# Kernel optimization log

Hardware: AMD Instinct MI355X
Metric: run time of the kernel (lower is better)

The kernel has to match this reference:

```python
import jax, jax.numpy as jnp
import numpy as np

S_LEN, T_LEN, BATCH, HID = 32, 32, 64, 512


def setup_inputs() -> dict:
    key = jax.random.key(0)
    ks = jax.random.split(key, 5)
    H = HID
    sc = lambda n: 1.0 / np.sqrt(n)
    return {
        "source": jax.random.normal(ks[0], (S_LEN, BATCH, H), jnp.float32),
        "target": jax.random.normal(ks[1], (T_LEN, BATCH, H), jnp.float32),
        # H2h Dense: concat(s_h, t_h) [B, 2H] -> [B, H], linear
        "W_H2h": (jax.random.normal(ks[2], (2 * H, H), jnp.float32) * sc(2 * H)),
        "b_H2h": jnp.zeros((H,), jnp.float32),
        # shared LSTMCell weights (Keras gate order i, f, g, o)
        "W_kernel": (jax.random.normal(ks[3], (H, 4 * H), jnp.float32) * sc(H)),
        "W_rec": (jax.random.normal(ks[4], (H, 4 * H), jnp.float32) * sc(H)),
        "b_lstm": jnp.zeros((4 * H,), jnp.float32),
    }


def _lstm_cell(x, h, c, Wk, Wr, b):
    # Keras LSTMCell math, gate order i, f, g(candidate), o
    z = x @ Wk + h @ Wr + b  # [B, 4H]
    i, f, g, o = jnp.split(z, 4, axis=-1)
    c2 = jax.nn.sigmoid(f) * c + jax.nn.sigmoid(i) * jnp.tanh(g)
    h2 = jax.nn.sigmoid(o) * jnp.tanh(c2)
    return h2, c2


def reference(source, target, W_H2h, b_H2h, W_kernel, W_rec, b_lstm):
    # source: [S, B, H] (time-major), target: [T, B, H]
    T, B, H = target.shape

    def inner(s_state, t_slice):
        # s_state carried along the target axis; t_slice is target cell j state
        s_step, s_h, s_m = s_state
        t_step, t_h, t_m = t_slice
        hmid = jnp.concatenate([s_h, t_h], axis=1) @ W_H2h + b_H2h  # [B, H]
        ns_h, ns_m = _lstm_cell(s_step, hmid, s_m, W_kernel, W_rec, b_lstm)
        nt_h, nt_m = _lstm_cell(t_step, hmid, t_m, W_kernel, W_rec, b_lstm)
        # step arrays get overwritten with the new hidden state
        return (ns_h, ns_h, ns_m), (nt_h, nt_h, nt_m)

    def outer(t_arrays, s_in):
        # fresh source state per outer step i: step = source[i], h = m = 0
        z = jnp.zeros_like(s_in)
        (s_step_f, _, _), t_new = jax.lax.scan(inner, (s_in, z, z), t_arrays)
        return t_new, s_step_f

    zeros = jnp.zeros((T, B, H), source.dtype)
    t_final, source_out = jax.lax.scan(outer, (target, zeros, zeros), source)
    return source_out, t_final[0]
```

## Files before the change

### kernel.cpp

```cpp
#include <hip/hip_runtime.h>

#define BLK 256

typedef __bf16 bf16;
typedef __bf16 bf16x8 __attribute__((ext_vector_type(8)));
typedef float f32x4 __attribute__((ext_vector_type(4)));

__device__ __forceinline__ float sigm(float x) { return 1.f / (1.f + __expf(-x)); }
__device__ __forceinline__ float tanh_(float x) {
    x = fminf(fmaxf(x, -15.f), 15.f);
    float e = __expf(2.f * x);
    return (e - 1.f) / (e + 1.f);
}

__device__ __forceinline__ void gl2lds(const bf16* g, bf16* l) {
    __builtin_amdgcn_global_load_lds((const __attribute__((address_space(1))) void*)g,
                                     (__attribute__((address_space(3))) void*)l, 16, 0, 0);
}

__global__ __launch_bounds__(256) void k_prep(
    const float* __restrict__ src, const float* __restrict__ tgt,
    const float* __restrict__ WH, const float* __restrict__ bH,
    const float* __restrict__ Wk, const float* __restrict__ Wr,
    const float* __restrict__ bl,
    bf16* __restrict__ srcb, bf16* __restrict__ tgtb,
    bf16* __restrict__ WHhi, bf16* __restrict__ WHlo,
    bf16* __restrict__ Wrhi, bf16* __restrict__ Wrlo,
    bf16* __restrict__ P2, float* __restrict__ bz) {
    __shared__ float tile[64][65];
    const int bid = blockIdx.x, t = threadIdx.x;
    if (bid < 512) {
        const float* in = (bid < 256) ? Wr : Wk;
        bf16* ohi = (bid < 256) ? Wrhi : P2;
        bf16* olo = (bid < 256) ? Wrlo : nullptr;
        const int b = bid & 255;
        const int tr = b >> 5, tc = b & 31;
#pragma unroll
        for (int q = 0; q < 16; q++) {
            int idx = q * 256 + t, lr = idx >> 6, lc = idx & 63;
            tile[lr][lc] = in[(size_t)(tr * 64 + lr) * 2048 + tc * 64 + lc];
        }
        __syncthreads();
#pragma unroll
        for (int q = 0; q < 16; q++) {
            int idx = q * 256 + t, lr = idx >> 6, lc = idx & 63;
            float v = tile[lc][lr];
            size_t o = (size_t)(tc * 64 + lr) * 512 + tr * 64 + lc;
            bf16 h = (bf16)v;
            ohi[o] = h;
            if (olo) olo[o] = (bf16)(v - (float)h);
        }
    } else if (bid < 520) {
        int c = (bid - 512) * 256 + t;
        float s = bl[c];
        for (int k = 0; k < 512; k++) s += bH[k] * Wr[(size_t)k * 2048 + c];
        bz[c] = s;
    } else {
        const int gt = (bid - 520) * 256 + t, NT = 504 * 256;
        for (int id = gt; id < 1048576; id += NT) srcb[id] = (bf16)src[id];
        for (int id = gt; id < 1048576; id += NT) tgtb[id] = (bf16)tgt[id];
        for (int id = gt; id < 524288; id += NT) {
            float v = WH[id];
            bf16 h = (bf16)v;
            WHhi[id] = h;
            WHlo[id] = (bf16)(v - (float)h);
        }
    }
}

__global__ __launch_bounds__(256, 4) void k_gemmP(
    const bf16* __restrict__ Wrhi, const bf16* __restrict__ Wrlo,
    const bf16* __restrict__ WHhi, const bf16* __restrict__ WHlo,
    bf16* __restrict__ P3, bf16* __restrict__ P4) {
    __shared__ __align__(16) bf16 At[64 * 64];
    __shared__ __align__(16) bf16 Bt[128 * 64];
    const int t = threadIdx.x, w = t >> 6, l = t & 63;
    const int m0 = (blockIdx.x >> 3) * 64, n0 = (blockIdx.x & 7) * 128;
    f32x4 acc[2][4] = {};
    const bf16* Aps[3] = {Wrhi, Wrlo, Wrhi};
    const bf16* Bps[3] = {WHhi, WHhi, WHlo};
    for (int ph = 0; ph < 3; ph++) {
        const bf16* Ap = Aps[ph] + (size_t)m0 * 512;
        const bf16* Bp = Bps[ph] + (size_t)n0 * 512;
        for (int kt = 0; kt < 8; kt++) {
            int k0 = kt * 64;
            __syncthreads();
#pragma unroll
            for (int q = 0; q < 2; q++) {
                int pp = q * 256 + t;
                int r = pp >> 3, c = (pp & 7) ^ (r & 7);
                gl2lds(Ap + (size_t)r * 512 + k0 + c * 8, &At[(q * 256 + w * 64) * 8]);
            }
#pragma unroll
            for (int q = 0; q < 4; q++) {
                int pp = q * 256 + t;
                int r = pp >> 3, c = (pp & 7) ^ (r & 7);
                gl2lds(Bp + (size_t)r * 512 + k0 + c * 8, &Bt[(q * 256 + w * 64) * 8]);
            }
            __syncthreads();
#pragma unroll
            for (int ks = 0; ks < 2; ks++) {
                int c = ks * 4 + (l >> 4);
                bf16x8 af[2], bb[4];
#pragma unroll
                for (int mt = 0; mt < 2; mt++) {
                    int r = (w >> 1) * 32 + mt * 16 + (l & 15);
                    af[mt] = *(const bf16x8*)&At[(r * 8 + (c ^ (r & 7))) * 8];
                }
#pragma unroll
                for (int g = 0; g < 4; g++) {
                    int r = g * 32 + (w & 1) * 16 + (l & 15);
                    bb[g] = *(const bf16x8*)&Bt[(r * 8 + (c ^ (r & 7))) * 8];
                }
#pragma unroll
                for (int mt = 0; mt < 2; mt++)
#pragma unroll
                    for (int g = 0; g < 4; g++)
                        acc[mt][g] = __builtin_amdgcn_mfma_f32_16x16x32_bf16(
                            af[mt], bb[g], acc[mt][g], 0, 0, 0);
            }
        }
    }
    const bool hihalf = (n0 >= 512);
#pragma unroll
    for (int mt = 0; mt < 2; mt++) {
#pragma unroll
        for (int g = 0; g < 4; g++) {
            int np = n0 + g * 32 + (w & 1) * 16 + (l & 15);
#pragma unroll
            for (int r = 0; r < 4; r++) {
                int c = m0 + (w >> 1) * 32 + mt * 16 + ((l >> 4) << 2) + r;
                float v = acc[mt][g][r];
                if (!hihalf) P4[(size_t)c * 512 + np] = (bf16)v;
                else P3[(size_t)c * 512 + (np - 512)] = (bf16)v;
            }
        }
    }
}

__global__ __launch_bounds__(256, 3) void k_diag7(
    int d, int i_lo, int Kd,
    const bf16* __restrict__ srcb, const bf16* __restrict__ tgtb,
    const bf16* __restrict__ P2, const bf16* __restrict__ P3,
    const bf16* __restrict__ P4,
    const float* __restrict__ bz,
    const bf16* __restrict__ shR, bf16* __restrict__ shW,
    const bf16* __restrict__ thR, bf16* __restrict__ thW,
    float* __restrict__ sc, float* __restrict__ tc,
    float* __restrict__ out) {
    __shared__ __align__(16) bf16 As[64 * 32];
    __shared__ __align__(16) bf16 At2[64 * 32];
    __shared__ __align__(16) bf16 Bk[128 * 32];
    __shared__ __align__(16) bf16 Bs[128 * 32];
    __shared__ __align__(16) bf16 Bt[128 * 32];
    const int t = threadIdx.x, w = t >> 6, l = t & 63;
    const int bid = blockIdx.x;
    const int xcd = bid & 7, idx = bid >> 3;
    const int ch0 = (xcd * 2 + (idx & 1)) << 5;
    const int cell = idx >> 1;
    const int i = i_lo + cell, j = d - i;
    const bool uS = (j > 0), uT = (i > 0);
    const size_t stI = (size_t)i * 32768, stJ = (size_t)j * 32768;

    const bf16* Asrc = (j == 0 ? srcb : shR) + stI;
    const bf16* Atsrc = (i == 0 ? tgtb : thR) + stJ;

    f32x4 accS[2][4] = {};
    f32x4 accT[2][4] = {};
    f32x4 accU[2][4] = {};

#pragma unroll 1
    for (int kt = 0; kt < 16; kt++) {
        const int k0 = kt * 32;
        __syncthreads();
        {
            int rA = t >> 2, cA = (t & 3) ^ (rA & 3);
            size_t soA = (size_t)rA * 512 + k0 + cA * 8;
            gl2lds(Asrc + soA, As + w * 512);
            gl2lds(Atsrc + soA, At2 + w * 512);
        }
#pragma unroll
        for (int q = 0; q < 2; q++) {
            int pp = q * 256 + t;
            int r = pp >> 2, c = (pp & 3) ^ (r & 3);
            size_t so = (size_t)((r >> 5) * 512 + ch0 + (r & 31)) * 512 + k0 + c * 8;
            int dsto = (q * 256 + w * 64) * 8;
            gl2lds(P2 + so, Bk + dsto);
            if (uS) gl2lds(P4 + so, Bs + dsto);
            if (uT) gl2lds(P3 + so, Bt + dsto);
        }
        __syncthreads();

        const int cq = l >> 4;
        bf16x8 aS[2], aT[2], bb[4];
#pragma unroll
        for (int mt = 0; mt < 2; mt++) {
            int r = (w >> 1) * 32 + mt * 16 + (l & 15);
            int co = (r * 4 + (cq ^ (r & 3))) * 8;
            aS[mt] = *(const bf16x8*)&As[co];
            aT[mt] = *(const bf16x8*)&At2[co];
        }
#pragma unroll
        for (int g = 0; g < 4; g++) {
            int r = g * 32 + (w & 1) * 16 + (l & 15);
            bb[g] = *(const bf16x8*)&Bk[(r * 4 + (cq ^ (r & 3))) * 8];
        }
#pragma unroll
        for (int mt = 0; mt < 2; mt++)
#pragma unroll
            for (int g = 0; g < 4; g++) {
                accS[mt][g] = __builtin_amdgcn_mfma_f32_16x16x32_bf16(
                    aS[mt], bb[g], accS[mt][g], 0, 0, 0);
                accT[mt][g] = __builtin_amdgcn_mfma_f32_16x16x32_bf16(
                    aT[mt], bb[g], accT[mt][g], 0, 0, 0);
            }
        if (uS) {
#pragma unroll
            for (int g = 0; g < 4; g++) {
                int r = g * 32 + (w & 1) * 16 + (l & 15);
                bb[g] = *(const bf16x8*)&Bs[(r * 4 + (cq ^ (r & 3))) * 8];
            }
#pragma unroll
            for (int mt = 0; mt < 2; mt++)
#pragma unroll
                for (int g = 0; g < 4; g++)
                    accU[mt][g] = __builtin_amdgcn_mfma_f32_16x16x32_bf16(
                        aS[mt], bb[g], accU[mt][g], 0, 0, 0);
        }
        if (uT) {
#pragma unroll
            for (int g = 0; g < 4; g++) {
                int r = g * 32 + (w & 1) * 16 + (l & 15);
                bb[g] = *(const bf16x8*)&Bt[(r * 4 + (cq ^ (r & 3))) * 8];
            }
#pragma unroll
            for (int mt = 0; mt < 2; mt++)
#pragma unroll
                for (int g = 0; g < 4; g++)
                    accU[mt][g] = __builtin_amdgcn_mfma_f32_16x16x32_bf16(
                        aT[mt], bb[g], accU[mt][g], 0, 0, 0);
        }
    }

    const int h = ch0 + (w & 1) * 16 + (l & 15);
    float bzv[4];
#pragma unroll
    for (int g = 0; g < 4; g++) bzv[g] = bz[g * 512 + h];
#pragma unroll
    for (int mt = 0; mt < 2; mt++) {
#pragma unroll
        for (int r = 0; r < 4; r++) {
            int b = (w >> 1) * 32 + mt * 16 + ((l >> 4) << 2) + r;
            float u0 = accU[mt][0][r], u1 = accU[mt][1][r];
            float u2 = accU[mt][2][r], u3 = accU[mt][3][r];
            {
                float zi = accS[mt][0][r] + u0 + bzv[0];
                float zf = accS[mt][1][r] + u1 + bzv[1];
                float zg = accS[mt][2][r] + u2 + bzv[2];
                float zo = accS[mt][3][r] + u3 + bzv[3];
                size_t off = stI + (size_t)b * 512 + h;
                float cold = uS ? sc[off] : 0.f;
                float c2 = sigm(zf) * cold + sigm(zi) * tanh_(zg);
                float h2 = sigm(zo) * tanh_(c2);
                sc[off] = c2;
                shW[off] = (bf16)h2;
                if (j == 31) out[off] = h2;
            }
            {
                float zi = accT[mt][0][r] + u0 + bzv[0];
                float zf = accT[mt][1][r] + u1 + bzv[1];
                float zg = accT[mt][2][r] + u2 + bzv[2];
                float zo = accT[mt][3][r] + u3 + bzv[3];
                size_t off = stJ + (size_t)b * 512 + h;
                float cold = uT ? tc[off] : 0.f;
                float c2 = sigm(zf) * cold + sigm(zi) * tanh_(zg);
                float h2 = sigm(zo) * tanh_(c2);
                tc[off] = c2;
                thW[off] = (bf16)h2;
                if (i == 31) out[1048576 + off] = h2;
            }
        }
    }
}


extern "C" void kernel_launch(void* const* d_in, const int* in_sizes, int n_in,
                              void* d_out, int out_size, void* d_ws, size_t ws_size,
                              hipStream_t stream) {
    char* w = (char*)d_ws;
    const size_t MB = 1u << 20;
    const float* src = (const float*)d_in[0];
    const float* tgt = (const float*)d_in[1];
    const float* WH = (const float*)d_in[2];
    const float* bH = (const float*)d_in[3];
    const float* Wk = (const float*)d_in[4];
    const float* Wr = (const float*)d_in[5];
    const float* bl = (const float*)d_in[6];
    float* out = (float*)d_out;

    bf16* srcb = (bf16*)(w + 0 * MB);
    bf16* tgtb = (bf16*)(w + 2 * MB);
    bf16* WHhi = (bf16*)(w + 4 * MB);
    bf16* WHlo = (bf16*)(w + 5 * MB);
    bf16* Wrhi = (bf16*)(w + 6 * MB);
    bf16* Wrlo = (bf16*)(w + 8 * MB);
    bf16* P2 = (bf16*)(w + 12 * MB);
    bf16* P3 = (bf16*)(w + 14 * MB);
    bf16* P4 = (bf16*)(w + 16 * MB);
    float* bz = (float*)(w + 20 * MB);
    bf16* sh = (bf16*)(w + 21 * MB);
    bf16* th = (bf16*)(w + 25 * MB);
    float* sc = (float*)(w + 29 * MB);
    float* tc = (float*)(w + 33 * MB);

    k_prep<<<1024, BLK, 0, stream>>>(src, tgt, WH, bH, Wk, Wr, bl, srcb, tgtb,
                                     WHhi, WHlo, Wrhi, Wrlo, P2, bz);
    k_gemmP<<<256, BLK, 0, stream>>>(Wrhi, Wrlo, WHhi, WHlo, P3, P4);

    for (int d = 0; d < 63; d++) {
        int i_lo = d > 31 ? d - 31 : 0;
        int i_hi = d < 31 ? d : 31;
        int Kd = i_hi - i_lo + 1;
        const bf16* shR = sh + (size_t)(d & 1) * 1048576;
        bf16* shW = sh + (size_t)((d + 1) & 1) * 1048576;
        const bf16* thR = th + (size_t)(d & 1) * 1048576;
        bf16* thW = th + (size_t)((d + 1) & 1) * 1048576;
        k_diag7<<<Kd * 16, BLK, 0, stream>>>(d, i_lo, Kd, srcb, tgtb, P2, P3, P4,
                                             bz, shR, shW, thR, thW, sc, tc, out);
    }
}
```

Measured before the change: 1.681 ms.

## Replace per-diagonal launches with persistent kernel using dataflow counters

The 63 per-diagonal kernel launches are replaced by one persistent kernel. It walks work items in wavefront order, and each item spin-waits on per-cell atomic counters until its source and target predecessors have finished. Counters are zeroed in the prep kernel, and the double-buffered hidden-state arrays are indexed by j and i parity rather than by diagonal. This aims to remove launch overhead and the global barrier between diagonals so cells can start as soon as their inputs are ready. The cost is spin-waiting, a risk of deadlock if not all blocks are resident, and possible hazards in reusing the ping-pong buffers.

New measurement: 2.925 ms. 1.74x slower.

```diff
diff --git a/kernel.cpp b/kernel.cpp
--- a/kernel.cpp
+++ b/kernel.cpp
@@ -1,6 +1,7 @@
 #include <hip/hip_runtime.h>
 
 #define BLK 256
+#define N_ITEMS 16384
 
 typedef __bf16 bf16;
 typedef __bf16 bf16x8 __attribute__((ext_vector_type(8)));
@@ -26,7 +27,7 @@
     bf16* __restrict__ srcb, bf16* __restrict__ tgtb,
     bf16* __restrict__ WHhi, bf16* __restrict__ WHlo,
     bf16* __restrict__ Wrhi, bf16* __restrict__ Wrlo,
-    bf16* __restrict__ P2, float* __restrict__ bz) {
+    bf16* __restrict__ P2, float* __restrict__ bz, int* __restrict__ cnt) {
     __shared__ float tile[64][65];
     const int bid = blockIdx.x, t = threadIdx.x;
     if (bid < 512) {
@@ -51,6 +52,8 @@
             if (olo) olo[o] = (bf16)(v - (float)h);
         }
     } else if (bid < 520) {
+        if (bid == 512)
+            for (int z = t; z < 1024; z += 256) cnt[z] = 0;
         int c = (bid - 512) * 256 + t;
         float s = bl[c];
         for (int k = 0; k < 512; k++) s += bH[k] * Wr[(size_t)k * 2048 + c];
@@ -138,148 +141,180 @@
     }
 }
 
-__global__ __launch_bounds__(256, 3) void k_diag7(
-    int d, int i_lo, int Kd,
+__global__ __launch_bounds__(256, 3) void k_persist(
     const bf16* __restrict__ srcb, const bf16* __restrict__ tgtb,
     const bf16* __restrict__ P2, const bf16* __restrict__ P3,
     const bf16* __restrict__ P4,
     const float* __restrict__ bz,
-    const bf16* __restrict__ shR, bf16* __restrict__ shW,
-    const bf16* __restrict__ thR, bf16* __restrict__ thW,
+    bf16* __restrict__ sh, bf16* __restrict__ th,
     float* __restrict__ sc, float* __restrict__ tc,
-    float* __restrict__ out) {
+    int* __restrict__ cnt, float* __restrict__ out) {
     __shared__ __align__(16) bf16 As[64 * 32];
     __shared__ __align__(16) bf16 At2[64 * 32];
     __shared__ __align__(16) bf16 Bk[128 * 32];
     __shared__ __align__(16) bf16 Bs[128 * 32];
     __shared__ __align__(16) bf16 Bt[128 * 32];
     const int t = threadIdx.x, w = t >> 6, l = t & 63;
-    const int bid = blockIdx.x;
-    const int xcd = bid & 7, idx = bid >> 3;
-    const int ch0 = (xcd * 2 + (idx & 1)) << 5;
-    const int cell = idx >> 1;
-    const int i = i_lo + cell, j = d - i;
-    const bool uS = (j > 0), uT = (i > 0);
-    const size_t stI = (size_t)i * 32768, stJ = (size_t)j * 32768;
-
-    const bf16* Asrc = (j == 0 ? srcb : shR) + stI;
-    const bf16* Atsrc = (i == 0 ? tgtb : thR) + stJ;
-
-    f32x4 accS[2][4] = {};
-    f32x4 accT[2][4] = {};
-    f32x4 accU[2][4] = {};
+    const int G = gridDim.x;
+
+    for (int item = blockIdx.x; item < N_ITEMS; item += G) {
+        const int c = item >> 4, ch0 = (item & 15) << 5;
+        int d = 0, st = 0, stPrev = 0;
+        for (;;) {
+            const int lo = d > 31 ? d - 31 : 0, hi = d < 31 ? d : 31;
+            const int Kd = hi - lo + 1;
+            if (c < st + Kd) break;
+            stPrev = st; st += Kd; ++d;
+        }
+        const int i = (d > 31 ? d - 31 : 0) + (c - st), j = d - i;
+        const bool uS = (j > 0), uT = (i > 0);
+
+        if (t == 0) {
+            const int lop = d > 32 ? d - 32 : 0;
+            if (uS) {
+                int* p = cnt + stPrev + (i - lop);
+                while (__hip_atomic_load(p, __ATOMIC_RELAXED, __HIP_MEMORY_SCOPE_AGENT) < 16)
+                    __builtin_amdgcn_s_sleep(2);
+                (void)__hip_atomic_load(p, __ATOMIC_ACQUIRE, __HIP_MEMORY_SCOPE_AGENT);
+            }
+            if (uT) {
+                int* p = cnt + stPrev + (i - 1 - lop);
+                while (__hip_atomic_load(p, __ATOMIC_RELAXED, __HIP_MEMORY_SCOPE_AGENT) < 16)
+                    __builtin_amdgcn_s_sleep(2);
+                (void)__hip_atomic_load(p, __ATOMIC_ACQUIRE, __HIP_MEMORY_SCOPE_AGENT);
+            }
+        }
+        __syncthreads();
+
+        const size_t stI = (size_t)i * 32768, stJ = (size_t)j * 32768;
+        const bf16* Asrc = (j == 0) ? srcb + stI
+                                    : sh + (size_t)((j & 1) ^ 1) * 1048576 + stI;
+        const bf16* Atsrc = (i == 0) ? tgtb + stJ
+                                     : th + (size_t)((i & 1) ^ 1) * 1048576 + stJ;
+        bf16* shW = sh + (size_t)(j & 1) * 1048576;
+        bf16* thW = th + (size_t)(i & 1) * 1048576;
+
+        f32x4 accS[2][4] = {};
+        f32x4 accT[2][4] = {};
+        f32x4 accU[2][4] = {};
 
 #pragma unroll 1
-    for (int kt = 0; kt < 16; kt++) {
-        const int k0 = kt * 32;
-        __syncthreads();
-        {
-            int rA = t >> 2, cA = (t & 3) ^ (rA & 3);
-            size_t soA = (size_t)rA * 512 + k0 + cA * 8;
-            gl2lds(Asrc + soA, As + w * 512);
-            gl2lds(Atsrc + soA, At2 + w * 512);
-        }
-#pragma unroll
-        for (int q = 0; q < 2; q++) {
-            int pp = q * 256 + t;
-            int r = pp >> 2, c = (pp & 3) ^ (r & 3);
-            size_t so = (size_t)((r >> 5) * 512 + ch0 + (r & 31)) * 512 + k0 + c * 8;
-            int dsto = (q * 256 + w * 64) * 8;
-            gl2lds(P2 + so, Bk + dsto);
-            if (uS) gl2lds(P4 + so, Bs + dsto);
-            if (uT) gl2lds(P3 + so, Bt + dsto);
-        }
-        __syncthreads();
-
-        const int cq = l >> 4;
-        bf16x8 aS[2], aT[2], bb[4];
-#pragma unroll
-        for (int mt = 0; mt < 2; mt++) {
-            int r = (w >> 1) * 32 + mt * 16 + (l & 15);
-            int co = (r * 4 + (cq ^ (r & 3))) * 8;
-            aS[mt] = *(const bf16x8*)&As[co];
-            aT[mt] = *(const bf16x8*)&At2[co];
-        }
-#pragma unroll
-        for (int g = 0; g < 4; g++) {
-            int r = g * 32 + (w & 1) * 16 + (l & 15);
-            bb[g] = *(const bf16x8*)&Bk[(r * 4 + (cq ^ (r & 3))) * 8];
-        }
-#pragma unroll
-        for (int mt = 0; mt < 2; mt++)
-#pragma unroll
-            for (int g = 0; g < 4; g++) {
-                accS[mt][g] = __builtin_amdgcn_mfma_f32_16x16x32_bf16(
-                    aS[mt], bb[g], accS[mt][g], 0, 0, 0);
-                accT[mt][g] = __builtin_amdgcn_mfma_f32_16x16x32_bf16(
-                    aT[mt], bb[g], accT[mt][g], 0, 0, 0);
-            }
-        if (uS) {
+        for (int kt = 0; kt < 16; kt++) {
+            const int k0 = kt * 32;
+            __syncthreads();
+            {
+                int rA = t >> 2, cA = (t & 3) ^ (rA & 3);
+                size_t soA = (size_t)rA * 512 + k0 + cA * 8;
+                gl2lds(Asrc + soA, As + w * 512);
+                gl2lds(Atsrc + soA, At2 + w * 512);
+            }
+#pragma unroll
+            for (int q = 0; q < 2; q++) {
+                int pp = q * 256 + t;
+                int r = pp >> 2, cc = (pp & 3) ^ (r & 3);
+                size_t so = (size_t)((r >> 5) * 512 + ch0 + (r & 31)) * 512 + k0 + cc * 8;
+                int dsto = (q * 256 + w * 64) * 8;
+                gl2lds(P2 + so, Bk + dsto);
+                if (uS) gl2lds(P4 + so, Bs + dsto);
+                if (uT) gl2lds(P3 + so, Bt + dsto);
+            }
+            __syncthreads();
+
+            const int cq = l >> 4;
+            bf16x8 aS[2], aT[2], bb[4];
+#pragma unroll
+            for (int mt = 0; mt < 2; mt++) {
+                int r = (w >> 1) * 32 + mt * 16 + (l & 15);
+                int co = (r * 4 + (cq ^ (r & 3))) * 8;
+                aS[mt] = *(const bf16x8*)&As[co];
+                aT[mt] = *(const bf16x8*)&At2[co];
+            }
 #pragma unroll
             for (int g = 0; g < 4; g++) {
                 int r = g * 32 + (w & 1) * 16 + (l & 15);
-                bb[g] = *(const bf16x8*)&Bs[(r * 4 + (cq ^ (r & 3))) * 8];
+                bb[g] = *(const bf16x8*)&Bk[(r * 4 + (cq ^ (r & 3))) * 8];
             }
 #pragma unroll
             for (int mt = 0; mt < 2; mt++)
 #pragma unroll
-                for (int g = 0; g < 4; g++)
-                    accU[mt][g] = __builtin_amdgcn_mfma_f32_16x16x32_bf16(
-                        aS[mt], bb[g], accU[mt][g], 0, 0, 0);
-        }
-        if (uT) {
-#pragma unroll
-            for (int g = 0; g < 4; g++) {
-                int r = g * 32 + (w & 1) * 16 + (l & 15);
-                bb[g] = *(const bf16x8*)&Bt[(r * 4 + (cq ^ (r & 3))) * 8];
-            }
-#pragma unroll
-            for (int mt = 0; mt < 2; mt++)
-#pragma unroll
-                for (int g = 0; g < 4; g++)
-                    accU[mt][g] = __builtin_amdgcn_mfma_f32_16x16x32_bf16(
-                        aT[mt], bb[g], accU[mt][g], 0, 0, 0);
-        }
-    }
-
-    const int h = ch0 + (w & 1) * 16 + (l & 15);
-    float bzv[4];
-#pragma unroll
-    for (int g = 0; g < 4; g++) bzv[g] = bz[g * 512 + h];
-#pragma unroll
-    for (int mt = 0; mt < 2; mt++) {
-#pragma unroll
-        for (int r = 0; r < 4; r++) {
-            int b = (w >> 1) * 32 + mt * 16 + ((l >> 4) << 2) + r;
-            float u0 = accU[mt][0][r], u1 = accU[mt][1][r];
-            float u2 = accU[mt][2][r], u3 = accU[mt][3][r];
-            {
-                float zi = accS[mt][0][r] + u0 + bzv[0];
-                float zf = accS[mt][1][r] + u1 + bzv[1];
-                float zg = accS[mt][2][r] + u2 + bzv[2];
-                float zo = accS[mt][3][r] + u3 + bzv[3];
-                size_t off = stI + (size_t)b * 512 + h;
-                float cold = uS ? sc[off] : 0.f;
-                float c2 = sigm(zf) * cold + sigm(zi) * tanh_(zg);
-                float h2 = sigm(zo) * tanh_(c2);
-                sc[off] = c2;
-                shW[off] = (bf16)h2;
-                if (j == 31) out[off] = h2;
-            }
-            {
-                float zi = accT[mt][0][r] + u0 + bzv[0];
-                float zf = accT[mt][1][r] + u1 + bzv[1];
-                float zg = accT[mt][2][r] + u2 + bzv[2];
-                float zo = accT[mt][3][r] + u3 + bzv[3];
-                size_t off = stJ + (size_t)b * 512 + h;
-                float cold = uT ? tc[off] : 0.f;
-                float c2 = sigm(zf) * cold + sigm(zi) * tanh_(zg);
-                float h2 = sigm(zo) * tanh_(c2);
-                tc[off] = c2;
-                thW[off] = (bf16)h2;
-                if (i == 31) out[1048576 + off] = h2;
-            }
-        }
+                for (int g = 0; g < 4; g++) {
+                    accS[mt][g] = __builtin_amdgcn_mfma_f32_16x16x32_bf16(
+                        aS[mt], bb[g], accS[mt][g], 0, 0, 0);
+                    accT[mt][g] = __builtin_amdgcn_mfma_f32_16x16x32_bf16(
+                        aT[mt], bb[g], accT[mt][g], 0, 0, 0);
+                }
+            if (uS) {
+#pragma unroll
+                for (int g = 0; g < 4; g++) {
+                    int r = g * 32 + (w & 1) * 16 + (l & 15);
+                    bb[g] = *(const bf16x8*)&Bs[(r * 4 + (cq ^ (r & 3))) * 8];
+                }
+#pragma unroll
+                for (int mt = 0; mt < 2; mt++)
+#pragma unroll
+                    for (int g = 0; g < 4; g++)
+                        accU[mt][g] = __builtin_amdgcn_mfma_f32_16x16x32_bf16(
+                            aS[mt], bb[g], accU[mt][g], 0, 0, 0);
+            }
+            if (uT) {
+#pragma unroll
+                for (int g = 0; g < 4; g++) {
+                    int r = g * 32 + (w & 1) * 16 + (l & 15);
+                    bb[g] = *(const bf16x8*)&Bt[(r * 4 + (cq ^ (r & 3))) * 8];
+                }
+#pragma unroll
+                for (int mt = 0; mt < 2; mt++)
+#pragma unroll
+                    for (int g = 0; g < 4; g++)
+                        accU[mt][g] = __builtin_amdgcn_mfma_f32_16x16x32_bf16(
+                            aT[mt], bb[g], accU[mt][g], 0, 0, 0);
+            }
+        }
+
+        const int h = ch0 + (w & 1) * 16 + (l & 15);
+        float bzv[4];
+#pragma unroll
+        for (int g = 0; g < 4; g++) bzv[g] = bz[g * 512 + h];
+#pragma unroll
+        for (int mt = 0; mt < 2; mt++) {
+#pragma unroll
+            for (int r = 0; r < 4; r++) {
+                int b = (w >> 1) * 32 + mt * 16 + ((l >> 4) << 2) + r;
+                float u0 = accU[mt][0][r], u1 = accU[mt][1][r];
+                float u2 = accU[mt][2][r], u3 = accU[mt][3][r];
+                {
+                    float zi = accS[mt][0][r] + u0 + bzv[0];
+                    float zf = accS[mt][1][r] + u1 + bzv[1];
+                    float zg = accS[mt][2][r] + u2 + bzv[2];
+                    float zo = accS[mt][3][r] + u3 + bzv[3];
+                    size_t off = stI + (size_t)b * 512 + h;
+                    float cold = uS ? sc[off] : 0.f;
+                    float c2 = sigm(zf) * cold + sigm(zi) * tanh_(zg);
+                    float h2 = sigm(zo) * tanh_(c2);
+                    sc[off] = c2;
+                    shW[off] = (bf16)h2;
+                    if (j == 31) out[off] = h2;
+                }
+                {
+                    float zi = accT[mt][0][r] + u0 + bzv[0];
+                    float zf = accT[mt][1][r] + u1 + bzv[1];
+                    float zg = accT[mt][2][r] + u2 + bzv[2];
+                    float zo = accT[mt][3][r] + u3 + bzv[3];
+                    size_t off = stJ + (size_t)b * 512 + h;
+                    float cold = uT ? tc[off] : 0.f;
+                    float c2 = sigm(zf) * cold + sigm(zi) * tanh_(zg);
+                    float h2 = sigm(zo) * tanh_(c2);
+                    tc[off] = c2;
+                    thW[off] = (bf16)h2;
+                    if (i == 31) out[1048576 + off] = h2;
+                }
+            }
+        }
+
+        asm volatile("s_waitcnt vmcnt(0)" ::: "memory");
+        __syncthreads();
+        if (t == 0)
+            __hip_atomic_fetch_add(&cnt[c], 1, __ATOMIC_RELEASE, __HIP_MEMORY_SCOPE_AGENT);
     }
 }
 
@@ -308,24 +343,31 @@
     bf16* P3 = (bf16*)(w + 14 * MB);
     bf16* P4 = (bf16*)(w + 16 * MB);
     float* bz = (float*)(w + 20 * MB);
+    int* cnt = (int*)(w + 20 * MB + 64 * 1024);
     bf16* sh = (bf16*)(w + 21 * MB);
     bf16* th = (bf16*)(w + 25 * MB);
     float* sc = (float*)(w + 29 * MB);
     float* tc = (float*)(w + 33 * MB);
 
+    static int G = 0;
+    if (G == 0) {
+        int dev = 0;
+        hipGetDevice(&dev);
+        hipDeviceProp_t prop;
+        int nCU = 256;
+        if (hipGetDeviceProperties(&prop, dev) == hipSuccess && prop.multiProcessorCount > 0)
+            nCU = prop.multiProcessorCount;
+        int nb = 0;
+        if (hipOccupancyMaxActiveBlocksPerMultiprocessor(&nb, k_persist, BLK, 0) != hipSuccess ||
+            nb < 1)
+            nb = 2;
+        G = nb * nCU;
+        if (G > N_ITEMS) G = N_ITEMS;
+    }
+
     k_prep<<<1024, BLK, 0, stream>>>(src, tgt, WH, bH, Wk, Wr, bl, srcb, tgtb,
-                                     WHhi, WHlo, Wrhi, Wrlo, P2, bz);
+                                     WHhi, WHlo, Wrhi, Wrlo, P2, bz, cnt);
     k_gemmP<<<256, BLK, 0, stream>>>(Wrhi, Wrlo, WHhi, WHlo, P3, P4);
-
-    for (int d = 0; d < 63; d++) {
-        int i_lo = d > 31 ? d - 31 : 0;
-        int i_hi = d < 31 ? d : 31;
-        int Kd = i_hi - i_lo + 1;
-        const bf16* shR = sh + (size_t)(d & 1) * 1048576;
-        bf16* shW = sh + (size_t)((d + 1) & 1) * 1048576;
-        const bf16* thR = th + (size_t)(d & 1) * 1048576;
-        bf16* thW = th + (size_t)((d + 1) & 1) * 1048576;
-        k_diag7<<<Kd * 16, BLK, 0, stream>>>(d, i_lo, Kd, srcb, tgtb, P2, P3, P4,
-                                             bz, shR, shW, thR, thW, sc, tc, out);
-    }
-}
+    k_persist<<<G, BLK, 0, stream>>>(srcb, tgtb, P2, P3, P4, bz, sh, th, sc, tc,
+                                     cnt, out);
+}
```
